# Optimization experiments

Hardware: AMD Instinct MI355X
Metric: run time of the kernel (lower is better)

Reference implementation:

```python
import jax, jax.numpy as jnp
import numpy as np

B, T, D = 2, 4096, 512
H = 8
HS = D // H  # 64
CTX = 4096


def setup_inputs() -> dict:
    key = jax.random.key(0)
    ks = jax.random.split(key, 10)
    s = lambda fan_in: fan_in ** -0.5
    x = jax.random.normal(ks[0], (B, T, D), dtype=jnp.float32)
    # per-head q/k/v projections (no bias), stacked over heads: [H, D, HS]
    Wq = jax.random.normal(ks[1], (H, D, HS), dtype=jnp.float32) * s(D)
    Wk = jax.random.normal(ks[2], (H, D, HS), dtype=jnp.float32) * s(D)
    Wv = jax.random.normal(ks[3], (H, D, HS), dtype=jnp.float32) * s(D)
    # output projection [D, D] + bias
    Wproj = jax.random.normal(ks[4], (D, D), dtype=jnp.float32) * s(D)
    bproj = jax.random.normal(ks[5], (D,), dtype=jnp.float32) * 0.01
    # feed-forward: D -> 4D -> D
    W1 = jax.random.normal(ks[6], (D, 4 * D), dtype=jnp.float32) * s(D)
    b1 = jax.random.normal(ks[7], (4 * D,), dtype=jnp.float32) * 0.01
    W2 = jax.random.normal(ks[8], (4 * D, D), dtype=jnp.float32) * s(4 * D)
    b2 = jax.random.normal(ks[9], (D,), dtype=jnp.float32) * 0.01
    return {"x": x, "Wq": Wq, "Wk": Wk, "Wv": Wv, "Wproj": Wproj,
            "bproj": bproj, "W1": W1, "b1": b1, "W2": W2, "b2": b2}


def reference(x, Wq, Wk, Wv, Wproj, bproj, W1, b1, W2, b2):
    Bx, Tx, Dx = x.shape
    scale = HS ** -0.5
    # multi-head causal self-attention (naive, full TxT scores as in source)
    q = jnp.einsum('btd,hde->bhte', x, Wq)
    k = jnp.einsum('btd,hde->bhte', x, Wk)
    v = jnp.einsum('btd,hde->bhte', x, Wv)
    wei = jnp.einsum('bhte,bhse->bhts', q, k) * scale  # [B,H,T,T]
    causal = jnp.tril(jnp.ones((Tx, Tx), dtype=bool))
    wei = jnp.where(causal, wei, -jnp.inf)
    wei = jax.nn.softmax(wei, axis=-1)
    attn = jnp.einsum('bhts,bhse->bhte', wei, v)  # [B,H,T,HS]
    # concat heads (cat along last dim == transpose+reshape of stacked heads)
    attn = attn.transpose(0, 2, 1, 3).reshape(Bx, Tx, Dx)
    sa_out = attn @ Wproj + bproj
    x = x + sa_out
    # feed-forward with residual
    h = jax.nn.relu(x @ W1 + b1)
    x = x + (h @ W2 + b2)
    return x
```

## Files before the change

### kernel.cpp

```cpp
#include <hip/hip_runtime.h>


typedef __attribute__((ext_vector_type(8))) short bf16x8;
typedef __attribute__((ext_vector_type(4))) float f32x4;
typedef __attribute__((ext_vector_type(16))) float f32x16;
typedef unsigned short u16;

__device__ __forceinline__ u16 f2bf(float f) {
  union { float f; unsigned int i; } u; u.f = f;
  unsigned int r = u.i + 0x7fffu + ((u.i >> 16) & 1u);
  return (u16)(r >> 16);
}
__device__ __forceinline__ float bf2f(u16 s) {
  union { unsigned int i; float f; } u; u.i = ((unsigned int)s) << 16;
  return u.f;
}
__device__ __forceinline__ void gload16(const void* g, void* l) {
  __builtin_amdgcn_global_load_lds((const __attribute__((address_space(1))) void*)g,
                                   (__attribute__((address_space(3))) void*)l,
                                   16, 0, 0);
}

__global__ void cast_x_kernel(const float4* __restrict__ in, ushort4* __restrict__ out, int n4) {
  int i = blockIdx.x * blockDim.x + threadIdx.x;
  if (i >= n4) return;
  float4 v = in[i];
  ushort4 o; o.x = f2bf(v.x); o.y = f2bf(v.y); o.z = f2bf(v.z); o.w = f2bf(v.w);
  out[i] = o;
}

__global__ void transpose_cast_kernel(const float* __restrict__ in, u16* __restrict__ out,
                                      int C, int ldo, long in_z, long out_z) {
  __shared__ float t[32][33];
  in += (long)blockIdx.z * in_z;
  out += (long)blockIdx.z * out_z;
  int c0 = blockIdx.x * 32, r0 = blockIdx.y * 32;
  int tx = threadIdx.x & 31, ty = threadIdx.x >> 5;
#pragma unroll
  for (int k = 0; k < 4; k++)
    t[ty + 8 * k][tx] = in[(long)(r0 + ty + 8 * k) * C + c0 + tx];
  __syncthreads();
#pragma unroll
  for (int k = 0; k < 4; k++)
    out[(long)(c0 + ty + 8 * k) * ldo + r0 + tx] = f2bf(t[tx][ty + 8 * k]);
}

__global__ void transpose_v_kernel(const u16* __restrict__ qkv, u16* __restrict__ vt) {
  __shared__ u16 t[32][33];
  int z = blockIdx.z;
  const u16* in = qkv + (long)(z >> 3) * 4096 * 1536 + 1024 + (z & 7) * 64;
  u16* out = vt + (long)z * 64 * 4096;
  int c0 = blockIdx.x * 32, r0 = blockIdx.y * 32;
  int tx = threadIdx.x & 31, ty = threadIdx.x >> 5;
#pragma unroll
  for (int k = 0; k < 4; k++)
    t[ty + 8 * k][tx] = in[(long)(r0 + ty + 8 * k) * 1536 + c0 + tx];
  __syncthreads();
#pragma unroll
  for (int k = 0; k < 4; k++)
    out[(long)(c0 + ty + 8 * k) * 4096 + r0 + tx] = t[tx][ty + 8 * k];
}

template <int MODE, int BN>
__global__ __launch_bounds__(256) void gemm_bt_kernel(
    const u16* __restrict__ A, const u16* __restrict__ Bt, void* __restrict__ Out,
    const float* __restrict__ bias, const float* __restrict__ resf,
    const u16* __restrict__ resb, int N, int K) {
  __shared__ __align__(16) char As[128 * 128];
  __shared__ __align__(16) char Bs[BN * 128];
  const int tid = threadIdx.x;
  const int lane = tid & 63, w = tid >> 6;
  const int l15 = lane & 15, l4 = lane >> 4;
  const long m0 = (long)blockIdx.y * 128;
  const long n0 = (long)blockIdx.x * BN;
  const int wm = (w >> 1) * 64, wn = (w & 1) * (BN / 2);
  const int NB = BN / 32;

  f32x4 acc[4][NB] = {};

  for (int kt = 0; kt < K; kt += 64) {
#pragma unroll
    for (int i = 0; i < 4; i++) {
      int basechunk = i * 256 + w * 64;
      int chunk = basechunk + lane;
      int row = chunk >> 3, c = chunk & 7;
      int sc = c ^ (row & 7);
      gload16(A + (m0 + row) * K + kt + sc * 8, As + basechunk * 16);
    }
#pragma unroll
    for (int i = 0; i < BN / 32; i++) {
      int basechunk = i * 256 + w * 64;
      int chunk = basechunk + lane;
      int row = chunk >> 3, c = chunk & 7;
      int sc = c ^ (row & 7);
      gload16(Bt + (n0 + row) * K + kt + sc * 8, Bs + basechunk * 16);
    }
    __syncthreads();
#pragma unroll
    for (int kk = 0; kk < 2; kk++) {
      bf16x8 a[4], b[NB];
#pragma unroll
      for (int m = 0; m < 4; m++) {
        int row = wm + m * 16 + l15;
        int ch = (kk * 4 + l4) ^ (row & 7);
        a[m] = *(const bf16x8*)(As + row * 128 + ch * 16);
      }
#pragma unroll
      for (int n = 0; n < NB; n++) {
        int row = wn + n * 16 + l15;
        int ch = (kk * 4 + l4) ^ (row & 7);
        b[n] = *(const bf16x8*)(Bs + row * 128 + ch * 16);
      }
#pragma unroll
      for (int m = 0; m < 4; m++)
#pragma unroll
        for (int n = 0; n < NB; n++)
          acc[m][n] = __builtin_amdgcn_mfma_f32_16x16x32_bf16(a[m], b[n], acc[m][n], 0, 0, 0);
    }
    __syncthreads();
  }

#pragma unroll
  for (int m = 0; m < 4; m++) {
#pragma unroll
    for (int n = 0; n < NB; n++) {
      long gcol = n0 + wn + n * 16 + l15;
#pragma unroll
      for (int r = 0; r < 4; r++) {
        long grow = m0 + wm + m * 16 + l4 * 4 + r;
        float v = acc[m][n][r];
        if (MODE == 0) {
          ((u16*)Out)[grow * N + gcol] = f2bf(v);
        } else if (MODE == 1) {
          v += bias[gcol] + resf[grow * N + gcol];
          ((u16*)Out)[grow * N + gcol] = f2bf(v);
        } else if (MODE == 2) {
          v += bias[gcol];
          v = v > 0.f ? v : 0.f;
          ((u16*)Out)[grow * N + gcol] = f2bf(v);
        } else {
          v += bias[gcol] + bf2f(resb[grow * N + gcol]);
          ((float*)Out)[grow * N + gcol] = v;
        }
      }
    }
  }
}

__global__ __launch_bounds__(256, 4) void attn_kernel(
    const u16* __restrict__ qkv, const u16* __restrict__ vt,
    float* __restrict__ pacc, float* __restrict__ pml) {
  __shared__ __align__(16) char Ks[2][64 * 128];
  __shared__ __align__(16) char Vs[2][64 * 128];
  const int tid = threadIdx.x;
  const int lane = tid & 63, w = tid >> 6;
  const int l31 = lane & 31, l5 = lane >> 5;

  const int g = blockIdx.x;
  const int a = g & 255, r = g >> 8;
  const int t = a >> 3;
  const int qt = (r & 1) ? 31 - t : t;
  const int bh = (a & 7) | (((r >> 1) & 1) << 3);
  const int half = r & 1;
  const int b = bh >> 3, h = bh & 7;
  const int qt0 = qt * 128;
  const int j0 = half ? qt + 1 : 0;
  const int j1 = half ? 2 * qt + 2 : qt + 1;
  const int jdiag = 2 * qt;
  const u16* qbase = qkv + (long)b * 4096 * 1536 + h * 64;
  const u16* kbase = qbase + 512;
  const u16* vtbase = vt + (long)bh * 64 * 4096;

  const int qrow_g = qt0 + w * 32 + l31;
  bf16x8 aq[4];
  {
    const u16* qp = qbase + (long)qrow_g * 1536 + l5 * 8;
#pragma unroll
    for (int kk = 0; kk < 4; kk++) aq[kk] = *(const bf16x8*)(qp + kk * 16);
  }

#pragma unroll
  for (int i = 0; i < 2; i++) {
    int basechunk = i * 256 + w * 64;
    int chunk = basechunk + lane;
    int row = chunk >> 3, c = chunk & 7;
    int sc = c ^ (row & 7);
    gload16(kbase + (long)(j0 * 64 + row) * 1536 + sc * 8, Ks[0] + basechunk * 16);
    gload16(vtbase + (long)row * 4096 + j0 * 64 + sc * 8, Vs[0] + basechunk * 16);
  }
  __syncthreads();

  f32x16 oacc[2] = {};
  float mi = -1e30f, li = 0.f;
  const float cexp = 0.18033688f;

  for (int j = j0; j < j1; ++j) {
    const int cur = (j - j0) & 1;
    if (j + 1 < j1) {
#pragma unroll
      for (int i = 0; i < 2; i++) {
        int basechunk = i * 256 + w * 64;
        int chunk = basechunk + lane;
        int row = chunk >> 3, c = chunk & 7;
        int sc = c ^ (row & 7);
        gload16(kbase + (long)((j + 1) * 64 + row) * 1536 + sc * 8, Ks[cur ^ 1] + basechunk * 16);
        gload16(vtbase + (long)row * 4096 + (j + 1) * 64 + sc * 8, Vs[cur ^ 1] + basechunk * 16);
      }
    }

    f32x16 st[2] = {};
#pragma unroll
    for (int kk = 0; kk < 4; kk++) {
      int ch = ((l5 + 2 * kk) ^ (l31 & 7)) * 16;
      bf16x8 ak0 = *(const bf16x8*)(Ks[cur] + l31 * 128 + ch);
      bf16x8 ak1 = *(const bf16x8*)(Ks[cur] + (32 + l31) * 128 + ch);
      st[0] = __builtin_amdgcn_mfma_f32_32x32x16_bf16(ak0, aq[kk], st[0], 0, 0, 0);
      st[1] = __builtin_amdgcn_mfma_f32_32x32x16_bf16(ak1, aq[kk], st[1], 0, 0, 0);
    }

    if (j >= jdiag) {
      int thr = qrow_g - j * 64;
#pragma unroll
      for (int n = 0; n < 2; n++)
#pragma unroll
        for (int reg = 0; reg < 16; reg++) {
          int key = n * 32 + 4 * l5 + (reg & 3) + 8 * (reg >> 2);
          if (key > thr) st[n][reg] = -1e30f;
        }
    }

    float pm = st[0][0];
#pragma unroll
    for (int n = 0; n < 2; n++)
#pragma unroll
      for (int reg = 0; reg < 16; reg++) pm = fmaxf(pm, st[n][reg]);
    pm = fmaxf(pm, __shfl_xor(pm, 32, 64));
    float mn = fmaxf(mi, pm);
    float alpha = exp2f((mi - mn) * cexp);
    mi = mn;
    float ps = 0.f;
#pragma unroll
    for (int n = 0; n < 2; n++)
#pragma unroll
      for (int reg = 0; reg < 16; reg++) {
        float p = exp2f((st[n][reg] - mn) * cexp);
        st[n][reg] = p;
        ps += p;
      }
    ps += __shfl_xor(ps, 32, 64);
    li = li * alpha + ps;
#pragma unroll
    for (int ne = 0; ne < 2; ne++)
#pragma unroll
      for (int reg = 0; reg < 16; reg++) oacc[ne][reg] *= alpha;

    unsigned pk[2][4][2];
#pragma unroll
    for (int n = 0; n < 2; n++)
#pragma unroll
      for (int gg = 0; gg < 4; gg++)
#pragma unroll
        for (int t2 = 0; t2 < 2; t2++) {
          float lo = st[n][gg * 4 + 2 * t2], hi = st[n][gg * 4 + 2 * t2 + 1];
          unsigned d;
          asm("v_cvt_pk_bf16_f32 %0, %1, %2" : "=v"(d) : "v"(lo), "v"(hi));
          pk[n][gg][t2] = d;
        }

    unsigned bfr[4][4];
#pragma unroll
    for (int n = 0; n < 2; n++)
#pragma unroll
      for (int jj = 0; jj < 2; jj++)
#pragma unroll
        for (int t2 = 0; t2 < 2; t2++) {
          unsigned own = l5 ? pk[n][2 * jj + 1][t2] : pk[n][2 * jj][t2];
          unsigned oth = l5 ? pk[n][2 * jj][t2] : pk[n][2 * jj + 1][t2];
          unsigned zx = __shfl_xor(oth, 32, 64);
          int s = 2 * n + jj;
          bfr[s][t2] = l5 ? zx : own;
          bfr[s][2 + t2] = l5 ? own : zx;
        }

#pragma unroll
    for (int s = 0; s < 4; s++) {
      union { unsigned u[4]; bf16x8 v; } bp;
#pragma unroll
      for (int tt = 0; tt < 4; tt++) bp.u[tt] = bfr[s][tt];
      int ch = ((l5 + 2 * s) ^ (l31 & 7)) * 16;
      bf16x8 av0 = *(const bf16x8*)(Vs[cur] + l31 * 128 + ch);
      bf16x8 av1 = *(const bf16x8*)(Vs[cur] + (32 + l31) * 128 + ch);
      oacc[0] = __builtin_amdgcn_mfma_f32_32x32x16_bf16(av0, bp.v, oacc[0], 0, 0, 0);
      oacc[1] = __builtin_amdgcn_mfma_f32_32x32x16_bf16(av1, bp.v, oacc[1], 0, 0, 0);
    }
    __syncthreads();
  }

  const int pidx = (bh * 32 + qt) * 2 + half;
  float* pa = pacc + (long)pidx * 8192;
#pragma unroll
  for (int ne = 0; ne < 2; ne++)
#pragma unroll
    for (int gg = 0; gg < 4; gg++) {
      float4 vv;
      vv.x = oacc[ne][4 * gg + 0];
      vv.y = oacc[ne][4 * gg + 1];
      vv.z = oacc[ne][4 * gg + 2];
      vv.w = oacc[ne][4 * gg + 3];
      *(float4*)(pa + (w * 32 + l31) * 64 + ne * 32 + 4 * l5 + 8 * gg) = vv;
    }
  if (l5 == 0) {
    float2 vv; vv.x = mi; vv.y = li;
    ((float2*)(pml + (long)pidx * 256))[w * 32 + l31] = vv;
  }
}

__global__ __launch_bounds__(256) void attn_merge_kernel(
    const float* __restrict__ pacc, const float* __restrict__ pml, u16* __restrict__ attnb) {
  int tile = blockIdx.x;
  int bh = tile >> 5, qt = tile & 31;
  int b = bh >> 3, h = bh & 7;
  const float* a0 = pacc + (long)tile * 2 * 8192;
  const float* a1 = a0 + 8192;
  const float2* ml0 = (const float2*)(pml + (long)tile * 2 * 256);
  const float2* ml1 = ml0 + 128;
  int t = threadIdx.x;
  int cg = (t & 15) * 4;
  int rsub = t >> 4;
#pragma unroll
  for (int pass = 0; pass < 8; ++pass) {
    int row = pass * 16 + rsub;
    float2 v0 = ml0[row], v1 = ml1[row];
    float M = fmaxf(v0.x, v1.x);
    float w0 = __expf((v0.x - M) * 0.125f);
    float w1 = __expf((v1.x - M) * 0.125f);
    float inv = 1.f / (v0.y * w0 + v1.y * w1);
    float4 x0 = *(const float4*)(a0 + row * 64 + cg);
    float4 x1 = *(const float4*)(a1 + row * 64 + cg);
    ushort4 o;
    o.x = f2bf((x0.x * w0 + x1.x * w1) * inv);
    o.y = f2bf((x0.y * w0 + x1.y * w1) * inv);
    o.z = f2bf((x0.z * w0 + x1.z * w1) * inv);
    o.w = f2bf((x0.w * w0 + x1.w * w1) * inv);
    *(ushort4*)(attnb + ((long)(b * 4096 + qt * 128 + row)) * 512 + h * 64 + cg) = o;
  }
}

extern "C" void kernel_launch(void* const* d_in, const int* in_sizes, int n_in,
                              void* d_out, int out_size, void* d_ws, size_t ws_size,
                              hipStream_t stream) {
  const float* x = (const float*)d_in[0];
  const float* Wq = (const float*)d_in[1];
  const float* Wk = (const float*)d_in[2];
  const float* Wv = (const float*)d_in[3];
  const float* Wproj = (const float*)d_in[4];
  const float* bproj = (const float*)d_in[5];
  const float* W1 = (const float*)d_in[6];
  const float* b1 = (const float*)d_in[7];
  const float* W2 = (const float*)d_in[8];
  const float* b2 = (const float*)d_in[9];

  char* ws = (char*)d_ws;
  u16* xb      = (u16*)(ws);
  u16* wqkv_t  = (u16*)(ws + 8388608);
  u16* wproj_t = (u16*)(ws + 9961472);
  u16* w1_t    = (u16*)(ws + 10485760);
  u16* w2_t    = (u16*)(ws + 12582912);
  u16* qkv     = (u16*)(ws + 14680064);
  u16* vt      = (u16*)(ws + 39845888);
  u16* attnb   = (u16*)(ws + 48234496);
  u16* x1b     = (u16*)(ws + 56623104);
  u16* hbuf    = (u16*)(ws + 65011712);
  float* pml   = (float*)(ws + 56623104 + 2097152);
  float* pacc  = (float*)(ws + 65011712);

  cast_x_kernel<<<4096, 256, 0, stream>>>((const float4*)x, (ushort4*)xb, 8192 * 512 / 4);

  transpose_cast_kernel<<<dim3(2, 16, 8), 256, 0, stream>>>(Wq, wqkv_t, 64, 512, 32768L, 32768L);
  transpose_cast_kernel<<<dim3(2, 16, 8), 256, 0, stream>>>(Wk, wqkv_t + 512 * 512, 64, 512, 32768L, 32768L);
  transpose_cast_kernel<<<dim3(2, 16, 8), 256, 0, stream>>>(Wv, wqkv_t + 1024 * 512, 64, 512, 32768L, 32768L);
  transpose_cast_kernel<<<dim3(16, 16, 1), 256, 0, stream>>>(Wproj, wproj_t, 512, 512, 0, 0);
  transpose_cast_kernel<<<dim3(64, 16, 1), 256, 0, stream>>>(W1, w1_t, 2048, 512, 0, 0);
  transpose_cast_kernel<<<dim3(16, 64, 1), 256, 0, stream>>>(W2, w2_t, 512, 2048, 0, 0);

  gemm_bt_kernel<0, 128><<<dim3(12, 64), 256, 0, stream>>>(xb, wqkv_t, qkv, nullptr, nullptr, nullptr, 1536, 512);
  transpose_v_kernel<<<dim3(2, 128, 16), 256, 0, stream>>>(qkv, vt);
  attn_kernel<<<1024, 256, 0, stream>>>(qkv, vt, pacc, pml);
  attn_merge_kernel<<<512, 256, 0, stream>>>(pacc, pml, attnb);
  gemm_bt_kernel<1, 64><<<dim3(8, 64), 256, 0, stream>>>(attnb, wproj_t, x1b, bproj, x, nullptr, 512, 512);
  gemm_bt_kernel<2, 128><<<dim3(16, 64), 256, 0, stream>>>(x1b, w1_t, hbuf, b1, nullptr, nullptr, 2048, 512);
  gemm_bt_kernel<3, 64><<<dim3(8, 64), 256, 0, stream>>>(hbuf, w2_t, d_out, b2, nullptr, x1b, 512, 2048);
}
```

Baseline: 223.3 us.

## Fuse attention tile pairs per block, lazy softmax rescale, permlane32 swaps

Each attention block now processes two complementary query-tile halves in sequence (tile t and tile 31-t), so the grid shrinks from 1024 to 512 blocks with balanced work per block. The online-softmax rescale of the accumulator and row sum is skipped unless some row max grows past a fixed threshold. Cross-half-wave exchanges switch from __shfl_xor to v_permlane32_swap. Max and sum reductions become trees, and MFMA sections are wrapped in s_setprio. Launch bounds drop to 2 waves per SIMD, which frees registers but can cut occupancy, and the fewer, longer blocks may fill the GPU less evenly.

```diff
diff --git a/kernel.cpp b/kernel.cpp
--- a/kernel.cpp
+++ b/kernel.cpp
@@ -19,6 +19,39 @@
   __builtin_amdgcn_global_load_lds((const __attribute__((address_space(1))) void*)g,
                                    (__attribute__((address_space(3))) void*)l,
                                    16, 0, 0);
+}
+
+__device__ __forceinline__ void plswap_u(unsigned &a, unsigned &b) {
+#if defined(__has_builtin) && __has_builtin(__builtin_amdgcn_permlane32_swap)
+  auto r = __builtin_amdgcn_permlane32_swap(a, b, false, false);
+  a = (unsigned)r[0]; b = (unsigned)r[1];
+#else
+  asm("v_permlane32_swap_b32 %0, %1" : "+v"(a), "+v"(b));
+#endif
+}
+__device__ __forceinline__ void plswap_f(float &a, float &b) {
+  unsigned ua = __builtin_bit_cast(unsigned, a), ub = __builtin_bit_cast(unsigned, b);
+  plswap_u(ua, ub);
+  a = __builtin_bit_cast(float, ua); b = __builtin_bit_cast(float, ub);
+}
+
+__device__ __forceinline__ float tmax16(const f32x16 v) {
+  float a = fmaxf(v[0], v[8]),  b = fmaxf(v[1], v[9]);
+  float c = fmaxf(v[2], v[10]), d = fmaxf(v[3], v[11]);
+  float e = fmaxf(v[4], v[12]), f = fmaxf(v[5], v[13]);
+  float g = fmaxf(v[6], v[14]), h = fmaxf(v[7], v[15]);
+  a = fmaxf(a, e); b = fmaxf(b, f); c = fmaxf(c, g); d = fmaxf(d, h);
+  a = fmaxf(a, c); b = fmaxf(b, d);
+  return fmaxf(a, b);
+}
+__device__ __forceinline__ float tsum16(const f32x16 v) {
+  float a = v[0] + v[8],  b = v[1] + v[9];
+  float c = v[2] + v[10], d = v[3] + v[11];
+  float e = v[4] + v[12], f = v[5] + v[13];
+  float g = v[6] + v[14], h = v[7] + v[15];
+  a += e; b += f; c += g; d += h;
+  a += c; b += d;
+  return a + b;
 }
 
 __global__ void cast_x_kernel(const float4* __restrict__ in, ushort4* __restrict__ out, int n4) {
@@ -147,7 +180,7 @@
   }
 }
 
-__global__ __launch_bounds__(256, 4) void attn_kernel(
+__global__ __launch_bounds__(256, 2) void attn_kernel(
     const u16* __restrict__ qkv, const u16* __restrict__ vt,
     float* __restrict__ pacc, float* __restrict__ pml) {
   __shared__ __align__(16) char Ks[2][64 * 128];
@@ -155,163 +188,160 @@
   const int tid = threadIdx.x;
   const int lane = tid & 63, w = tid >> 6;
   const int l31 = lane & 31, l5 = lane >> 5;
+  const float cexp = 0.18033688f;
 
   const int g = blockIdx.x;
-  const int a = g & 255, r = g >> 8;
-  const int t = a >> 3;
-  const int qt = (r & 1) ? 31 - t : t;
-  const int bh = (a & 7) | (((r >> 1) & 1) << 3);
-  const int half = r & 1;
-  const int b = bh >> 3, h = bh & 7;
-  const int qt0 = qt * 128;
-  const int j0 = half ? qt + 1 : 0;
-  const int j1 = half ? 2 * qt + 2 : qt + 1;
-  const int jdiag = 2 * qt;
+  const int bh = g & 15, b = bh >> 3, h = bh & 7;
   const u16* qbase = qkv + (long)b * 4096 * 1536 + h * 64;
   const u16* kbase = qbase + 512;
   const u16* vtbase = vt + (long)bh * 64 * 4096;
 
-  const int qrow_g = qt0 + w * 32 + l31;
-  bf16x8 aq[4];
-  {
-    const u16* qp = qbase + (long)qrow_g * 1536 + l5 * 8;
-#pragma unroll
-    for (int kk = 0; kk < 4; kk++) aq[kk] = *(const bf16x8*)(qp + kk * 16);
-  }
-
-#pragma unroll
-  for (int i = 0; i < 2; i++) {
-    int basechunk = i * 256 + w * 64;
-    int chunk = basechunk + lane;
-    int row = chunk >> 3, c = chunk & 7;
-    int sc = c ^ (row & 7);
-    gload16(kbase + (long)(j0 * 64 + row) * 1536 + sc * 8, Ks[0] + basechunk * 16);
-    gload16(vtbase + (long)row * 4096 + j0 * 64 + sc * 8, Vs[0] + basechunk * 16);
-  }
-  __syncthreads();
-
-  f32x16 oacc[2] = {};
-  float mi = -1e30f, li = 0.f;
-  const float cexp = 0.18033688f;
-
-  for (int j = j0; j < j1; ++j) {
-    const int cur = (j - j0) & 1;
-    if (j + 1 < j1) {
-#pragma unroll
-      for (int i = 0; i < 2; i++) {
-        int basechunk = i * 256 + w * 64;
-        int chunk = basechunk + lane;
-        int row = chunk >> 3, c = chunk & 7;
-        int sc = c ^ (row & 7);
-        gload16(kbase + (long)((j + 1) * 64 + row) * 1536 + sc * 8, Ks[cur ^ 1] + basechunk * 16);
-        gload16(vtbase + (long)row * 4096 + (j + 1) * 64 + sc * 8, Vs[cur ^ 1] + basechunk * 16);
-      }
-    }
-
-    f32x16 st[2] = {};
-#pragma unroll
-    for (int kk = 0; kk < 4; kk++) {
-      int ch = ((l5 + 2 * kk) ^ (l31 & 7)) * 16;
-      bf16x8 ak0 = *(const bf16x8*)(Ks[cur] + l31 * 128 + ch);
-      bf16x8 ak1 = *(const bf16x8*)(Ks[cur] + (32 + l31) * 128 + ch);
-      st[0] = __builtin_amdgcn_mfma_f32_32x32x16_bf16(ak0, aq[kk], st[0], 0, 0, 0);
-      st[1] = __builtin_amdgcn_mfma_f32_32x32x16_bf16(ak1, aq[kk], st[1], 0, 0, 0);
-    }
-
-    if (j >= jdiag) {
-      int thr = qrow_g - j * 64;
+  for (int it = 0; it < 2; ++it) {
+    const int qt = it ? 31 - (g >> 4) : (g >> 4);
+    const int half = it;
+    const int qt0 = qt * 128;
+    const int j0 = half ? qt + 1 : 0;
+    const int j1 = half ? 2 * qt + 2 : qt + 1;
+    const int jdiag = 2 * qt;
+
+    const int qrow_g = qt0 + w * 32 + l31;
+    bf16x8 aq[4];
+    {
+      const u16* qp = qbase + (long)qrow_g * 1536 + l5 * 8;
+#pragma unroll
+      for (int kk = 0; kk < 4; kk++) aq[kk] = *(const bf16x8*)(qp + kk * 16);
+    }
+
+#pragma unroll
+    for (int i = 0; i < 2; i++) {
+      int basechunk = i * 256 + w * 64;
+      int chunk = basechunk + lane;
+      int row = chunk >> 3, c = chunk & 7;
+      int sc = c ^ (row & 7);
+      gload16(kbase + (long)(j0 * 64 + row) * 1536 + sc * 8, Ks[0] + basechunk * 16);
+      gload16(vtbase + (long)row * 4096 + j0 * 64 + sc * 8, Vs[0] + basechunk * 16);
+    }
+    __syncthreads();
+
+    f32x16 oacc[2] = {};
+    float mi = -1e30f, li = 0.f;
+
+    for (int j = j0; j < j1; ++j) {
+      const int cur = (j - j0) & 1;
+      if (j + 1 < j1) {
+#pragma unroll
+        for (int i = 0; i < 2; i++) {
+          int basechunk = i * 256 + w * 64;
+          int chunk = basechunk + lane;
+          int row = chunk >> 3, c = chunk & 7;
+          int sc = c ^ (row & 7);
+          gload16(kbase + (long)((j + 1) * 64 + row) * 1536 + sc * 8, Ks[cur ^ 1] + basechunk * 16);
+          gload16(vtbase + (long)row * 4096 + (j + 1) * 64 + sc * 8, Vs[cur ^ 1] + basechunk * 16);
+        }
+      }
+
+      f32x16 st[2] = {};
+      __builtin_amdgcn_s_setprio(1);
+#pragma unroll
+      for (int kk = 0; kk < 4; kk++) {
+        int ch = ((l5 + 2 * kk) ^ (l31 & 7)) * 16;
+        bf16x8 ak0 = *(const bf16x8*)(Ks[cur] + l31 * 128 + ch);
+        bf16x8 ak1 = *(const bf16x8*)(Ks[cur] + (32 + l31) * 128 + ch);
+        st[0] = __builtin_amdgcn_mfma_f32_32x32x16_bf16(ak0, aq[kk], st[0], 0, 0, 0);
+        st[1] = __builtin_amdgcn_mfma_f32_32x32x16_bf16(ak1, aq[kk], st[1], 0, 0, 0);
+      }
+      __builtin_amdgcn_s_setprio(0);
+
+      if (j >= jdiag) {
+        int thr = qrow_g - j * 64;
+#pragma unroll
+        for (int n = 0; n < 2; n++)
+#pragma unroll
+          for (int reg = 0; reg < 16; reg++) {
+            int key = n * 32 + 4 * l5 + (reg & 3) + 8 * (reg >> 2);
+            if (key > thr) st[n][reg] = -1e30f;
+          }
+      }
+
+      float pm = fmaxf(tmax16(st[0]), tmax16(st[1]));
+      {
+        float ta = pm, tb = pm;
+        plswap_f(ta, tb);
+        pm = fmaxf(ta, tb);
+      }
+      if (__any(pm > mi + 44.3614f)) {
+        float mn = fmaxf(mi, pm);
+        float alpha = exp2f((mi - mn) * cexp);
+        mi = mn;
+        li *= alpha;
+#pragma unroll
+        for (int ne = 0; ne < 2; ne++)
+#pragma unroll
+          for (int reg = 0; reg < 16; reg++) oacc[ne][reg] *= alpha;
+      }
 #pragma unroll
       for (int n = 0; n < 2; n++)
 #pragma unroll
-        for (int reg = 0; reg < 16; reg++) {
-          int key = n * 32 + 4 * l5 + (reg & 3) + 8 * (reg >> 2);
-          if (key > thr) st[n][reg] = -1e30f;
-        }
-    }
-
-    float pm = st[0][0];
-#pragma unroll
-    for (int n = 0; n < 2; n++)
-#pragma unroll
-      for (int reg = 0; reg < 16; reg++) pm = fmaxf(pm, st[n][reg]);
-    pm = fmaxf(pm, __shfl_xor(pm, 32, 64));
-    float mn = fmaxf(mi, pm);
-    float alpha = exp2f((mi - mn) * cexp);
-    mi = mn;
-    float ps = 0.f;
-#pragma unroll
-    for (int n = 0; n < 2; n++)
-#pragma unroll
-      for (int reg = 0; reg < 16; reg++) {
-        float p = exp2f((st[n][reg] - mn) * cexp);
-        st[n][reg] = p;
-        ps += p;
-      }
-    ps += __shfl_xor(ps, 32, 64);
-    li = li * alpha + ps;
+        for (int reg = 0; reg < 16; reg++)
+          st[n][reg] = exp2f((st[n][reg] - mi) * cexp);
+      float ps = tsum16(st[0]) + tsum16(st[1]);
+      {
+        float ta = ps, tb = ps;
+        plswap_f(ta, tb);
+        ps = ta + tb;
+      }
+      li += ps;
+
+      unsigned bfr[4][4];
+#pragma unroll
+      for (int n = 0; n < 2; n++)
+#pragma unroll
+        for (int jj = 0; jj < 2; jj++)
+#pragma unroll
+          for (int t2 = 0; t2 < 2; t2++) {
+            float lo0 = st[n][(2 * jj) * 4 + 2 * t2], hi0 = st[n][(2 * jj) * 4 + 2 * t2 + 1];
+            float lo1 = st[n][(2 * jj + 1) * 4 + 2 * t2], hi1 = st[n][(2 * jj + 1) * 4 + 2 * t2 + 1];
+            unsigned pa, pb;
+            asm("v_cvt_pk_bf16_f32 %0, %1, %2" : "=v"(pa) : "v"(lo0), "v"(hi0));
+            asm("v_cvt_pk_bf16_f32 %0, %1, %2" : "=v"(pb) : "v"(lo1), "v"(hi1));
+            plswap_u(pa, pb);
+            bfr[2 * n + jj][t2] = pa;
+            bfr[2 * n + jj][2 + t2] = pb;
+          }
+
+      __builtin_amdgcn_s_setprio(1);
+#pragma unroll
+      for (int s = 0; s < 4; s++) {
+        union { unsigned u[4]; bf16x8 v; } bp;
+#pragma unroll
+        for (int tt = 0; tt < 4; tt++) bp.u[tt] = bfr[s][tt];
+        int ch = ((l5 + 2 * s) ^ (l31 & 7)) * 16;
+        bf16x8 av0 = *(const bf16x8*)(Vs[cur] + l31 * 128 + ch);
+        bf16x8 av1 = *(const bf16x8*)(Vs[cur] + (32 + l31) * 128 + ch);
+        oacc[0] = __builtin_amdgcn_mfma_f32_32x32x16_bf16(av0, bp.v, oacc[0], 0, 0, 0);
+        oacc[1] = __builtin_amdgcn_mfma_f32_32x32x16_bf16(av1, bp.v, oacc[1], 0, 0, 0);
+      }
+      __builtin_amdgcn_s_setprio(0);
+      __syncthreads();
+    }
+
+    const int pidx = (bh * 32 + qt) * 2 + half;
+    float* pa = pacc + (long)pidx * 8192;
 #pragma unroll
     for (int ne = 0; ne < 2; ne++)
 #pragma unroll
-      for (int reg = 0; reg < 16; reg++) oacc[ne][reg] *= alpha;
-
-    unsigned pk[2][4][2];
-#pragma unroll
-    for (int n = 0; n < 2; n++)
-#pragma unroll
-      for (int gg = 0; gg < 4; gg++)
-#pragma unroll
-        for (int t2 = 0; t2 < 2; t2++) {
-          float lo = st[n][gg * 4 + 2 * t2], hi = st[n][gg * 4 + 2 * t2 + 1];
-          unsigned d;
-          asm("v_cvt_pk_bf16_f32 %0, %1, %2" : "=v"(d) : "v"(lo), "v"(hi));
-          pk[n][gg][t2] = d;
-        }
-
-    unsigned bfr[4][4];
-#pragma unroll
-    for (int n = 0; n < 2; n++)
-#pragma unroll
-      for (int jj = 0; jj < 2; jj++)
-#pragma unroll
-        for (int t2 = 0; t2 < 2; t2++) {
-          unsigned own = l5 ? pk[n][2 * jj + 1][t2] : pk[n][2 * jj][t2];
-          unsigned oth = l5 ? pk[n][2 * jj][t2] : pk[n][2 * jj + 1][t2];
-          unsigned zx = __shfl_xor(oth, 32, 64);
-          int s = 2 * n + jj;
-          bfr[s][t2] = l5 ? zx : own;
-          bfr[s][2 + t2] = l5 ? own : zx;
-        }
-
-#pragma unroll
-    for (int s = 0; s < 4; s++) {
-      union { unsigned u[4]; bf16x8 v; } bp;
-#pragma unroll
-      for (int tt = 0; tt < 4; tt++) bp.u[tt] = bfr[s][tt];
-      int ch = ((l5 + 2 * s) ^ (l31 & 7)) * 16;
-      bf16x8 av0 = *(const bf16x8*)(Vs[cur] + l31 * 128 + ch);
-      bf16x8 av1 = *(const bf16x8*)(Vs[cur] + (32 + l31) * 128 + ch);
-      oacc[0] = __builtin_amdgcn_mfma_f32_32x32x16_bf16(av0, bp.v, oacc[0], 0, 0, 0);
-      oacc[1] = __builtin_amdgcn_mfma_f32_32x32x16_bf16(av1, bp.v, oacc[1], 0, 0, 0);
-    }
-    __syncthreads();
-  }
-
-  const int pidx = (bh * 32 + qt) * 2 + half;
-  float* pa = pacc + (long)pidx * 8192;
-#pragma unroll
-  for (int ne = 0; ne < 2; ne++)
-#pragma unroll
-    for (int gg = 0; gg < 4; gg++) {
-      float4 vv;
-      vv.x = oacc[ne][4 * gg + 0];
-      vv.y = oacc[ne][4 * gg + 1];
-      vv.z = oacc[ne][4 * gg + 2];
-      vv.w = oacc[ne][4 * gg + 3];
-      *(float4*)(pa + (w * 32 + l31) * 64 + ne * 32 + 4 * l5 + 8 * gg) = vv;
-    }
-  if (l5 == 0) {
-    float2 vv; vv.x = mi; vv.y = li;
-    ((float2*)(pml + (long)pidx * 256))[w * 32 + l31] = vv;
+      for (int gg = 0; gg < 4; gg++) {
+        float4 vv;
+        vv.x = oacc[ne][4 * gg + 0];
+        vv.y = oacc[ne][4 * gg + 1];
+        vv.z = oacc[ne][4 * gg + 2];
+        vv.w = oacc[ne][4 * gg + 3];
+        *(float4*)(pa + (w * 32 + l31) * 64 + ne * 32 + 4 * l5 + 8 * gg) = vv;
+      }
+    if (l5 == 0) {
+      float2 vv; vv.x = mi; vv.y = li;
+      ((float2*)(pml + (long)pidx * 256))[w * 32 + l31] = vv;
+    }
   }
 }
 
@@ -385,7 +415,7 @@
 
   gemm_bt_kernel<0, 128><<<dim3(12, 64), 256, 0, stream>>>(xb, wqkv_t, qkv, nullptr, nullptr, nullptr, 1536, 512);
   transpose_v_kernel<<<dim3(2, 128, 16), 256, 0, stream>>>(qkv, vt);
-  attn_kernel<<<1024, 256, 0, stream>>>(qkv, vt, pacc, pml);
+  attn_kernel<<<512, 256, 0, stream>>>(qkv, vt, pacc, pml);
   attn_merge_kernel<<<512, 256, 0, stream>>>(pacc, pml, attnb);
   gemm_bt_kernel<1, 64><<<dim3(8, 64), 256, 0, stream>>>(attnb, wproj_t, x1b, bproj, x, nullptr, 512, 512);
   gemm_bt_kernel<2, 128><<<dim3(16, 64), 256, 0, stream>>>(x1b, w1_t, hbuf, b1, nullptr, nullptr, 2048, 512);
```

Measured after the change: 221.9 us. Within noise of the previous version (-0.6%).
